# Kernel optimization log

Hardware: AMD Instinct MI355X
Metric: run time of the kernel (lower is better)

## Reference

```python
import jax, jax.numpy as jnp
import numpy as np

K = 8        # num capsules
DD = 64      # per-capsule dim (delta_d)
D = K * DD   # 512
T = 16384    # num target nodes (segments)
NB = 100000  # num neighbor nodes
E = 131072   # num edges
ROUIT = 3
BETA = 0.5


def seg_softmax(p, seg, num):
    # softmax over entries sharing the same segment id (axis 0)
    m = jax.lax.stop_gradient(jax.ops.segment_max(p, seg, num_segments=num))
    e = jnp.exp(p - m[seg])
    s = jax.ops.segment_sum(e, seg, num_segments=num)
    return e / s[seg]


def l2norm(x):
    # F.normalize along last axis with eps=1e-12
    n = jnp.sqrt(jnp.sum(x * x, axis=-1, keepdims=True))
    return x / jnp.maximum(n, 1e-12)


def setup_inputs() -> dict:
    key = jax.random.key(0)
    ks = jax.random.split(key, 9)
    return {
        "x_nb": jax.random.normal(ks[0], (NB, 512), dtype=jnp.float32),
        "ppr": jax.random.uniform(ks[1], (E,), dtype=jnp.float32),
        "pca_w": jax.random.normal(ks[2], (512, D), dtype=jnp.float32) * 0.02,
        "pca_b": jnp.zeros((D,), dtype=jnp.float32),
        "mlp_w": jax.random.normal(ks[3], (D, 40), dtype=jnp.float32) * 0.02,
        "mlp_b": jnp.zeros((40,), dtype=jnp.float32),
        "row_idx": jnp.sort(jax.random.randint(ks[4], (E,), 0, T, dtype=jnp.int32)),
        "col_idx": jax.random.randint(ks[5], (E,), 0, NB, dtype=jnp.int32),
        "x_idx": jax.random.randint(ks[6], (T,), 0, NB, dtype=jnp.int32),
    }


def reference(x_nb, ppr, pca_w, pca_b, mlp_w, mlp_b, row_idx, col_idx, x_idx):
    # pca projection + relu
    x = jax.nn.relu(x_nb @ pca_w + pca_b)            # (NB, D)
    # segment softmax of ppr over targets
    ppr = seg_softmax(ppr, row_idx, T)               # (E,)
    # is_xNorm: per-capsule l2 normalization
    x = l2norm(x.reshape(-1, K, DD)).reshape(-1, D)
    z = x[col_idx]                                   # (E, D) gathered neighbors
    zk = z.reshape(-1, K, DD)                        # (E, K, DD)
    # init_mtd == 2: ppr-weighted scatter-sum init
    u = jax.ops.segment_sum(z * ppr[:, None], row_idx, num_segments=T)  # (T, D)
    for it in range(ROUIT):
        uk = u[row_idx].reshape(-1, K, DD)           # (E, K, DD)
        p = jnp.einsum('ekd,ekd->ek', uk, zk)        # (E, K) capsule logits
        # attention == 1: segment softmax then blend with ppr
        p = seg_softmax(p, row_idx, T)
        p = BETA * p + (1.0 - BETA) * ppr[:, None]
        # final segment softmax
        p = seg_softmax(p, row_idx, T)
        u = jax.ops.segment_sum(zk * p[:, :, None], row_idx, num_segments=T)  # (T, K, DD)
        if it < ROUIT - 1:
            u = l2norm(u)
        u = u.reshape(T, D)
    out = jax.nn.relu(u)                             # dropout is identity at eval
    logits = out @ mlp_w + mlp_b                     # (T, nclass)
    return jax.nn.log_softmax(logits, axis=1)
```

## Files before the change

kernel.cpp:

```cpp
#include <hip/hip_runtime.h>
#include <cstdint>
#include <cstddef>

#define NB_N 100000
#define E_N  131072
#define T_N  16384
#define D_N  512
#define NCLS 40
#define NTILES 782
#define CAPR 12

typedef unsigned short u16;
typedef unsigned int   u32;
typedef __attribute__((ext_vector_type(8))) short  short8;
typedef __attribute__((ext_vector_type(4))) float  floatx4;

__device__ __forceinline__ u16 f2bf(float f) {
  u32 u = __float_as_uint(f);
  return (u16)((u + 0x7fffu + ((u >> 16) & 1u)) >> 16);
}
__device__ __forceinline__ void unpack8(uint4 z, float* f) {
  f[0] = __uint_as_float(z.x << 16);
  f[1] = __uint_as_float(z.x & 0xffff0000u);
  f[2] = __uint_as_float(z.y << 16);
  f[3] = __uint_as_float(z.y & 0xffff0000u);
  f[4] = __uint_as_float(z.z << 16);
  f[5] = __uint_as_float(z.z & 0xffff0000u);
  f[6] = __uint_as_float(z.w << 16);
  f[7] = __uint_as_float(z.w & 0xffff0000u);
}
__device__ __forceinline__ void gload_lds16(const void* g, void* s) {
  __builtin_amdgcn_global_load_lds(
      (const __attribute__((address_space(1))) unsigned int*)g,
      (__attribute__((address_space(3))) unsigned int*)s, 16, 0, 0);
}

__global__ void conv_bt(const float* __restrict__ w, u16* __restrict__ Bt) {
  int i = blockIdx.x * 256 + threadIdx.x;
  int n = i >> 9, k = i & 511;
  Bt[i] = f2bf(w[k * 512 + n]);
}

__global__ void conv_bt2(const float* __restrict__ w, u16* __restrict__ Bt2) {
  int i = blockIdx.x * 256 + threadIdx.x;
  int n = i >> 9, k = i & 511;
  Bt2[i] = (n < NCLS) ? f2bf(w[k * NCLS + n]) : (u16)0;
}

__global__ void conv_a(const float* __restrict__ A, u16* __restrict__ Ab) {
  int i = blockIdx.x * 256 + threadIdx.x;
  if (i >= NTILES * 128 * 128) return;
  int row = i >> 7;
  float4 v;
  if (row < NB_N) v = ((const float4*)(A + (size_t)row * 512))[i & 127];
  else            v = make_float4(0.f, 0.f, 0.f, 0.f);
  uint2 pk;
  pk.x = (u32)f2bf(v.x) | ((u32)f2bf(v.y) << 16);
  pk.y = (u32)f2bf(v.z) | ((u32)f2bf(v.w) << 16);
  *(uint2*)(Ab + (size_t)i * 4) = pk;
}

__global__ void build_offs(const int* __restrict__ rowi, int* __restrict__ offs) {
  int e = blockIdx.x * 256 + threadIdx.x;
  if (e >= E_N) return;
  int r  = rowi[e];
  int rp = (e == 0) ? -1 : rowi[e - 1];
  for (int t = rp + 1; t <= r; ++t) offs[t] = e;
  if (e == E_N - 1)
    for (int t = r + 1; t <= T_N; ++t) offs[t] = E_N;
}

__global__ void ppr_sm(const float* __restrict__ ppr, const int* __restrict__ offs,
                       float* __restrict__ pprn) {
  int t = blockIdx.x * 256 + threadIdx.x;
  int s = offs[t], en = offs[t + 1];
  if (s >= en) return;
  float m = -INFINITY;
  for (int e = s; e < en; ++e) m = fmaxf(m, ppr[e]);
  float sum = 0.f;
  for (int e = s; e < en; ++e) sum += expf(ppr[e] - m);
  float inv = 1.f / sum;
  for (int e = s; e < en; ++e) pprn[e] = expf(ppr[e] - m) * inv;
}

__global__ __launch_bounds__(256) void gemm_pca(
    const u16*   __restrict__ Ab,
    const u16*   __restrict__ Bt,
    const float* __restrict__ bias,
    u16*         __restrict__ xn) {
  __shared__ u16 SMEM[2 * 128 * 64];
  u16* As = SMEM;
  u16* Bs = SMEM + 128 * 64;
  const int tid  = threadIdx.x;
  const int wid  = tid >> 6, lane = tid & 63;
  const int quad = lane >> 4, l16 = lane & 15;
  const int b  = blockIdx.x;
  const int mt = (b & 7) | ((b >> 5) << 3);
  if (mt >= NTILES) return;
  const int m0 = mt * 128;
  const int n0 = ((b >> 3) & 3) * 128;
  const int wm = (wid >> 1) * 64;
  const int wn = (wid & 1) * 64;
  const int sw = l16 & 7;
  const u16* Arow = Ab + (size_t)m0 * 512;

  floatx4 acc[4][4];
#pragma unroll
  for (int i = 0; i < 4; ++i)
#pragma unroll
    for (int j = 0; j < 4; ++j) acc[i][j] = (floatx4){0.f, 0.f, 0.f, 0.f};

  for (int k0 = 0; k0 < 512; k0 += 64) {
#pragma unroll
    for (int j = 0; j < 4; ++j) {
      int ci  = j * 256 + wid * 64 + lane;
      int row = ci >> 3;
      int kcs = (lane & 7) ^ ((lane >> 3) & 7);
      gload_lds16(Arow + (size_t)row * 512 + k0 + kcs * 8,
                  &As[(size_t)(j * 256 + wid * 64) * 8]);
      gload_lds16(Bt + (size_t)(n0 + row) * 512 + k0 + kcs * 8,
                  &Bs[(size_t)(j * 256 + wid * 64) * 8]);
    }
    __syncthreads();
#pragma unroll
    for (int kk = 0; kk < 64; kk += 32) {
      short8 af[4], bf[4];
#pragma unroll
      for (int mi = 0; mi < 4; ++mi) {
        int c = (kk >> 3) + quad;
        af[mi] = *(const short8*)(&As[(wm + mi * 16 + l16) * 64 + ((c ^ sw) << 3)]);
      }
#pragma unroll
      for (int ni = 0; ni < 4; ++ni) {
        int c = (kk >> 3) + quad;
        bf[ni] = *(const short8*)(&Bs[(wn + ni * 16 + l16) * 64 + ((c ^ sw) << 3)]);
      }
#pragma unroll
      for (int mi = 0; mi < 4; ++mi)
#pragma unroll
        for (int ni = 0; ni < 4; ++ni)
          acc[mi][ni] = __builtin_amdgcn_mfma_f32_16x16x32_bf16(af[mi], bf[ni],
                                                                acc[mi][ni], 0, 0, 0);
    }
    __syncthreads();
  }

  u16* Os = SMEM;
#pragma unroll
  for (int mi = 0; mi < 4; ++mi) {
#pragma unroll
    for (int r = 0; r < 4; ++r) {
      int lrow = wm + mi * 16 + quad * 4 + r;
      float v[4];
      float ss = 0.f;
#pragma unroll
      for (int ni = 0; ni < 4; ++ni) {
        int n  = n0 + wn + ni * 16 + l16;
        float x = acc[mi][ni][r] + bias[n];
        x = fmaxf(x, 0.f);
        v[ni] = x;
        ss += x * x;
      }
      ss += __shfl_xor(ss, 1);
      ss += __shfl_xor(ss, 2);
      ss += __shfl_xor(ss, 4);
      ss += __shfl_xor(ss, 8);
      float sc = 1.f / fmaxf(sqrtf(ss), 1e-12f);
#pragma unroll
      for (int ni = 0; ni < 4; ++ni)
        Os[lrow * 128 + wn + ni * 16 + l16] = f2bf(v[ni] * sc);
    }
  }
  __syncthreads();
#pragma unroll
  for (int c8 = 0; c8 < 8; ++c8) {
    int idx = c8 * 256 + tid;
    int row = idx >> 4, chk = idx & 15;
    int gm = m0 + row;
    if (gm < NB_N) {
      uint4 val = *(const uint4*)(&Os[row * 128 + chk * 8]);
      *(uint4*)(xn + (size_t)gm * 512 + n0 + chk * 8) = val;
    }
  }
}

__global__ __launch_bounds__(256, 3) void fused_all(
    const u16* __restrict__ xn, const int* __restrict__ coli,
    const int* __restrict__ offs, const float* __restrict__ pprn,
    u16* __restrict__ ub) {
  const int lane = threadIdx.x & 63;
  const int t = blockIdx.x * 4 + (threadIdx.x >> 6);
  const int s = offs[t], en = offs[t + 1];
  int deg = en - s;
  if (deg > 64) deg = 64;
  const int cap = lane >> 3;
  const int slot = lane >> 3;

  int   mycol = (lane < deg) ? coli[s + lane] : 0;
  float myppr = (lane < deg) ? pprn[s + lane] : 0.f;

  uint4 zreg[CAPR];
#pragma unroll
  for (int j = 0; j < CAPR; ++j) {
    if (j < deg) {
      int c = __shfl(mycol, j);
      zreg[j] = *(const uint4*)(xn + (size_t)c * 512 + lane * 8);
    }
  }

  float uf[8] = {0.f, 0.f, 0.f, 0.f, 0.f, 0.f, 0.f, 0.f};
#pragma unroll
  for (int j = 0; j < CAPR; ++j) {
    if (j < deg) {
      float w = __shfl(myppr, j);
      float zf[8];
      unpack8(zreg[j], zf);
#pragma unroll
      for (int q = 0; q < 8; ++q) uf[q] += w * zf[q];
    }
  }
  for (int j = CAPR; j < deg; ++j) {
    float w = __shfl(myppr, j);
    int c = __shfl(mycol, j);
    uint4 zz = *(const uint4*)(xn + (size_t)c * 512 + lane * 8);
    float zf[8];
    unpack8(zz, zf);
#pragma unroll
    for (int q = 0; q < 8; ++q) uf[q] += w * zf[q];
  }

  float Preg[8];

  for (int it = 0; it < 3; ++it) {
#pragma unroll
    for (int j = 0; j < CAPR; ++j) {
      if (j < deg) {
        float zf[8];
        unpack8(zreg[j], zf);
        float d = uf[0]*zf[0] + uf[1]*zf[1] + uf[2]*zf[2] + uf[3]*zf[3] +
                  uf[4]*zf[4] + uf[5]*zf[5] + uf[6]*zf[6] + uf[7]*zf[7];
        d += __shfl_xor(d, 1);
        d += __shfl_xor(d, 2);
        d += __shfl_xor(d, 4);
        float dc = __shfl(d, (lane & 7) << 3);
        if (slot == (j & 7)) Preg[j >> 3] = dc;
      }
    }
    for (int j = CAPR; j < deg; ++j) {
      int c = __shfl(mycol, j);
      uint4 zz = *(const uint4*)(xn + (size_t)c * 512 + lane * 8);
      float zf[8];
      unpack8(zz, zf);
      float d = uf[0]*zf[0] + uf[1]*zf[1] + uf[2]*zf[2] + uf[3]*zf[3] +
                uf[4]*zf[4] + uf[5]*zf[5] + uf[6]*zf[6] + uf[7]*zf[7];
      d += __shfl_xor(d, 1);
      d += __shfl_xor(d, 2);
      d += __shfl_xor(d, 4);
      float dc = __shfl(d, (lane & 7) << 3);
      if (slot == (j & 7)) {
        int hi = j >> 3;
        if      (hi == 1) Preg[1] = dc;
        else if (hi == 2) Preg[2] = dc;
        else if (hi == 3) Preg[3] = dc;
        else if (hi == 4) Preg[4] = dc;
        else if (hi == 5) Preg[5] = dc;
        else if (hi == 6) Preg[6] = dc;
        else if (hi == 7) Preg[7] = dc;
      }
    }

    {
      float m1 = -INFINITY;
#pragma unroll
      for (int i = 0; i < 8; ++i)
        m1 = (slot + 8*i < deg) ? fmaxf(m1, Preg[i]) : m1;
      m1 = fmaxf(m1, __shfl_xor(m1, 8));
      m1 = fmaxf(m1, __shfl_xor(m1, 16));
      m1 = fmaxf(m1, __shfl_xor(m1, 32));
      float s1 = 0.f;
#pragma unroll
      for (int i = 0; i < 8; ++i)
        s1 += (slot + 8*i < deg) ? expf(Preg[i] - m1) : 0.f;
      s1 += __shfl_xor(s1, 8);
      s1 += __shfl_xor(s1, 16);
      s1 += __shfl_xor(s1, 32);
      float inv1 = 1.f / s1;
      float m2 = -INFINITY;
#pragma unroll
      for (int i = 0; i < 8; ++i) {
        int j = slot + 8*i;
        if (j < deg) {
          float pj = __shfl(myppr, j);
          float v = 0.5f * expf(Preg[i] - m1) * inv1 + 0.5f * pj;
          Preg[i] = v;
          m2 = fmaxf(m2, v);
        }
      }
      m2 = fmaxf(m2, __shfl_xor(m2, 8));
      m2 = fmaxf(m2, __shfl_xor(m2, 16));
      m2 = fmaxf(m2, __shfl_xor(m2, 32));
      float s2 = 0.f;
#pragma unroll
      for (int i = 0; i < 8; ++i)
        s2 += (slot + 8*i < deg) ? expf(Preg[i] - m2) : 0.f;
      s2 += __shfl_xor(s2, 8);
      s2 += __shfl_xor(s2, 16);
      s2 += __shfl_xor(s2, 32);
      float inv2 = 1.f / s2;
#pragma unroll
      for (int i = 0; i < 8; ++i)
        if (slot + 8*i < deg) Preg[i] = expf(Preg[i] - m2) * inv2;
    }

    float acc[8] = {0.f, 0.f, 0.f, 0.f, 0.f, 0.f, 0.f, 0.f};
#pragma unroll
    for (int j = 0; j < CAPR; ++j) {
      if (j < deg) {
        float w = __shfl(Preg[j >> 3], ((j & 7) << 3) | cap);
        float zf[8];
        unpack8(zreg[j], zf);
#pragma unroll
        for (int q = 0; q < 8; ++q) acc[q] += w * zf[q];
      }
    }
    for (int j = CAPR; j < deg; ++j) {
      int hi = j >> 3;
      float pr = Preg[1];
      if      (hi == 2) pr = Preg[2];
      else if (hi == 3) pr = Preg[3];
      else if (hi == 4) pr = Preg[4];
      else if (hi == 5) pr = Preg[5];
      else if (hi == 6) pr = Preg[6];
      else if (hi == 7) pr = Preg[7];
      float w = __shfl(pr, ((j & 7) << 3) | cap);
      int c = __shfl(mycol, j);
      uint4 zz = *(const uint4*)(xn + (size_t)c * 512 + lane * 8);
      float zf[8];
      unpack8(zz, zf);
#pragma unroll
      for (int q = 0; q < 8; ++q) acc[q] += w * zf[q];
    }
    if (it < 2) {
      float ss = 0.f;
#pragma unroll
      for (int q = 0; q < 8; ++q) ss += acc[q] * acc[q];
      ss += __shfl_xor(ss, 1);
      ss += __shfl_xor(ss, 2);
      ss += __shfl_xor(ss, 4);
      float sc = 1.f / fmaxf(sqrtf(ss), 1e-12f);
#pragma unroll
      for (int q = 0; q < 8; ++q) acc[q] *= sc;
    }
#pragma unroll
    for (int q = 0; q < 8; ++q) uf[q] = acc[q];
  }

  uint4 pk;
  pk.x = (u32)f2bf(fmaxf(uf[0], 0.f)) | ((u32)f2bf(fmaxf(uf[1], 0.f)) << 16);
  pk.y = (u32)f2bf(fmaxf(uf[2], 0.f)) | ((u32)f2bf(fmaxf(uf[3], 0.f)) << 16);
  pk.z = (u32)f2bf(fmaxf(uf[4], 0.f)) | ((u32)f2bf(fmaxf(uf[5], 0.f)) << 16);
  pk.w = (u32)f2bf(fmaxf(uf[6], 0.f)) | ((u32)f2bf(fmaxf(uf[7], 0.f)) << 16);
  *(uint4*)(ub + (size_t)t * 512 + lane * 8) = pk;
}

__global__ __launch_bounds__(256) void mlp_gemm(
    const u16* __restrict__ ub, const u16* __restrict__ Bt2,
    const float* __restrict__ mb, float* __restrict__ out) {
  const int wid = threadIdx.x >> 6, lane = threadIdx.x & 63;
  const int quad = lane >> 4, l16 = lane & 15;
  const int m0 = blockIdx.x * 64 + wid * 16;

  floatx4 acc[4];
#pragma unroll
  for (int ni = 0; ni < 4; ++ni) acc[ni] = (floatx4){0.f, 0.f, 0.f, 0.f};

#pragma unroll 4
  for (int kk = 0; kk < 512; kk += 32) {
    short8 af = *(const short8*)(ub + (size_t)(m0 + l16) * 512 + kk + quad * 8);
#pragma unroll
    for (int ni = 0; ni < 4; ++ni) {
      short8 bf = *(const short8*)(Bt2 + (size_t)(ni * 16 + l16) * 512 + kk + quad * 8);
      acc[ni] = __builtin_amdgcn_mfma_f32_16x16x32_bf16(af, bf, acc[ni], 0, 0, 0);
    }
  }

#pragma unroll
  for (int r = 0; r < 4; ++r) {
    int t = m0 + quad * 4 + r;
    float v[4];
    float mx = -INFINITY;
#pragma unroll
    for (int ni = 0; ni < 4; ++ni) {
      int c = ni * 16 + l16;
      float lg = (c < NCLS) ? (acc[ni][r] + mb[c]) : -INFINITY;
      v[ni] = lg;
      mx = fmaxf(mx, lg);
    }
    mx = fmaxf(mx, __shfl_xor(mx, 1));
    mx = fmaxf(mx, __shfl_xor(mx, 2));
    mx = fmaxf(mx, __shfl_xor(mx, 4));
    mx = fmaxf(mx, __shfl_xor(mx, 8));
    float se = 0.f;
#pragma unroll
    for (int ni = 0; ni < 4; ++ni) {
      int c = ni * 16 + l16;
      if (c < NCLS) se += expf(v[ni] - mx);
    }
    se += __shfl_xor(se, 1);
    se += __shfl_xor(se, 2);
    se += __shfl_xor(se, 4);
    se += __shfl_xor(se, 8);
    float lse = mx + logf(se);
#pragma unroll
    for (int ni = 0; ni < 4; ++ni) {
      int c = ni * 16 + l16;
      if (c < NCLS) out[(size_t)t * NCLS + c] = v[ni] - lse;
    }
  }
}

extern "C" void kernel_launch(void* const* d_in, const int* in_sizes, int n_in,
                              void* d_out, int out_size, void* d_ws, size_t ws_size,
                              hipStream_t stream) {
  const float* x_nb  = (const float*)d_in[0];
  const float* ppr   = (const float*)d_in[1];
  const float* pca_w = (const float*)d_in[2];
  const float* pca_b = (const float*)d_in[3];
  const float* mlp_w = (const float*)d_in[4];
  const float* mlp_b = (const float*)d_in[5];
  const int* row_idx = (const int*)d_in[6];
  const int* col_idx = (const int*)d_in[7];
  float* out = (float*)d_out;

  char* ws = (char*)d_ws;
  const size_t OFF_BT   = 0;
  const size_t OFF_PPRN = 512 * 1024;
  const size_t OFF_OFFS = 1024 * 1024;
  const size_t OFF_XN   = 1024 * 1024 + 128 * 1024;
  const size_t OFF_AB   = OFF_XN + (size_t)NB_N * 512 * 2;
  const size_t OFF_UB   = OFF_AB + (size_t)NTILES * 128 * 512 * 2;
  u16*   Bt   = (u16*)(ws + OFF_BT);
  u16*   Bt2  = (u16*)(ws + OFF_BT);
  float* pprn = (float*)(ws + OFF_PPRN);
  int*   offs = (int*)(ws + OFF_OFFS);
  u16*   xn   = (u16*)(ws + OFF_XN);
  u16*   Ab   = (u16*)(ws + OFF_AB);
  u16*   ub   = (u16*)(ws + OFF_UB);

  conv_bt<<<1024, 256, 0, stream>>>(pca_w, Bt);
  build_offs<<<512, 256, 0, stream>>>(row_idx, offs);
  ppr_sm<<<64, 256, 0, stream>>>(ppr, offs, pprn);

  conv_a<<<(NTILES * 128 * 128 + 255) / 256, 256, 0, stream>>>(x_nb, Ab);
  gemm_pca<<<98 * 32, 256, 0, stream>>>(Ab, Bt, pca_b, xn);
  conv_bt2<<<128, 256, 0, stream>>>(mlp_w, Bt2);

  fused_all<<<T_N / 4, 256, 0, stream>>>(xn, col_idx, offs, pprn, ub);

  mlp_gemm<<<256, 256, 0, stream>>>(ub, Bt2, mlp_b, out);
}
```

Before: 540.8 us.

## Run routing on per-capsule Gram matrices via MFMA for low-degree targets

For targets with at most 16 neighbors, the kernel now builds a per-capsule 16x16 Gram matrix of neighbor features with bf16 MFMA, stages it in LDS, and runs all three routing iterations as small matrix-vector products on coefficients. The norm of u is computed from the Gram matrix, so the final u is formed once from gathered z. This replaces repeated 64-dim dot products and weighted sums per iteration. High-degree targets keep the old path, and blocks shrink to two waves with LDS scratch. The Gram entries come from bf16 products, so rounding differs slightly, and the extra LDS use may limit occupancy.

```diff
diff --git a/kernel.cpp b/kernel.cpp
--- a/kernel.cpp
+++ b/kernel.cpp
@@ -184,175 +184,289 @@
   }
 }
 
-__global__ __launch_bounds__(256, 3) void fused_all(
+__device__ __forceinline__ void matvec16(const float (&g0)[16], const float (&g1)[16],
+                                         float w0, float w1, int base,
+                                         float& e0, float& e1) {
+  e0 = 0.f; e1 = 0.f;
+#pragma unroll
+  for (int j = 0; j < 8; ++j) {
+    float wj = __shfl(w0, base | j);
+    e0 += g0[j] * wj;
+    e1 += g1[j] * wj;
+  }
+#pragma unroll
+  for (int j = 0; j < 8; ++j) {
+    float wj = __shfl(w1, base | j);
+    e0 += g0[8 + j] * wj;
+    e1 += g1[8 + j] * wj;
+  }
+}
+
+__device__ __forceinline__ void segsm2(float& d0, float& d1, bool v0, bool v1) {
+  float m = fmaxf(v0 ? d0 : -INFINITY, v1 ? d1 : -INFINITY);
+  m = fmaxf(m, __shfl_xor(m, 1));
+  m = fmaxf(m, __shfl_xor(m, 2));
+  m = fmaxf(m, __shfl_xor(m, 4));
+  float e0 = v0 ? expf(d0 - m) : 0.f;
+  float e1 = v1 ? expf(d1 - m) : 0.f;
+  float s = e0 + e1;
+  s += __shfl_xor(s, 1);
+  s += __shfl_xor(s, 2);
+  s += __shfl_xor(s, 4);
+  float inv = 1.f / s;
+  d0 = e0 * inv;
+  d1 = e1 * inv;
+}
+
+__global__ __launch_bounds__(128, 4) void fused_all(
     const u16* __restrict__ xn, const int* __restrict__ coli,
     const int* __restrict__ offs, const float* __restrict__ pprn,
     u16* __restrict__ ub) {
+  __shared__ __align__(16) float Glds[2][8 * 260];
   const int lane = threadIdx.x & 63;
-  const int t = blockIdx.x * 4 + (threadIdx.x >> 6);
+  const int wv = threadIdx.x >> 6;
+  const int t = blockIdx.x * 2 + wv;
   const int s = offs[t], en = offs[t + 1];
   int deg = en - s;
   if (deg > 64) deg = 64;
-  const int cap = lane >> 3;
-  const int slot = lane >> 3;
 
   int   mycol = (lane < deg) ? coli[s + lane] : 0;
   float myppr = (lane < deg) ? pprn[s + lane] : 0.f;
 
-  uint4 zreg[CAPR];
-#pragma unroll
-  for (int j = 0; j < CAPR; ++j) {
-    if (j < deg) {
-      int c = __shfl(mycol, j);
-      zreg[j] = *(const uint4*)(xn + (size_t)c * 512 + lane * 8);
-    }
-  }
-
   float uf[8] = {0.f, 0.f, 0.f, 0.f, 0.f, 0.f, 0.f, 0.f};
-#pragma unroll
-  for (int j = 0; j < CAPR; ++j) {
-    if (j < deg) {
-      float w = __shfl(myppr, j);
-      float zf[8];
-      unpack8(zreg[j], zf);
-#pragma unroll
-      for (int q = 0; q < 8; ++q) uf[q] += w * zf[q];
-    }
-  }
-  for (int j = CAPR; j < deg; ++j) {
-    float w = __shfl(myppr, j);
-    int c = __shfl(mycol, j);
-    uint4 zz = *(const uint4*)(xn + (size_t)c * 512 + lane * 8);
-    float zf[8];
-    unpack8(zz, zf);
-#pragma unroll
-    for (int q = 0; q < 8; ++q) uf[q] += w * zf[q];
-  }
-
-  float Preg[8];
-
-  for (int it = 0; it < 3; ++it) {
+
+  if (deg <= 16) {
+    float* G = Glds[wv];
+    const int esrc = lane & 15, kq = lane >> 4;
+    int ce = __shfl(mycol, esrc);
+    const u16* zb = xn + (size_t)ce * 512 + kq * 8;
+    floatx4 gram[8];
+#pragma unroll
+    for (int c = 0; c < 8; ++c) {
+      short8 f0 = *(const short8*)(zb + c * 64);
+      short8 f1 = *(const short8*)(zb + c * 64 + 32);
+      floatx4 gg = (floatx4){0.f, 0.f, 0.f, 0.f};
+      gg = __builtin_amdgcn_mfma_f32_16x16x32_bf16(f0, f0, gg, 0, 0, 0);
+      gg = __builtin_amdgcn_mfma_f32_16x16x32_bf16(f1, f1, gg, 0, 0, 0);
+      gram[c] = gg;
+    }
+#pragma unroll
+    for (int c = 0; c < 8; ++c)
+      *(float4*)&G[c * 260 + esrc * 16 + kq * 4] = *(float4*)&gram[c];
+    const int cc = lane >> 3, i0 = lane & 7;
+    const int base = lane & 56;
+    float g0[16], g1[16];
+    {
+      const float* r0 = &G[cc * 260 + i0 * 16];
+      const float* r1 = &G[cc * 260 + (i0 + 8) * 16];
+#pragma unroll
+      for (int ch = 0; ch < 4; ++ch) {
+        float4 a = *(const float4*)(r0 + ch * 4);
+        float4 b = *(const float4*)(r1 + ch * 4);
+        g0[ch * 4 + 0] = a.x; g0[ch * 4 + 1] = a.y;
+        g0[ch * 4 + 2] = a.z; g0[ch * 4 + 3] = a.w;
+        g1[ch * 4 + 0] = b.x; g1[ch * 4 + 1] = b.y;
+        g1[ch * 4 + 2] = b.z; g1[ch * 4 + 3] = b.w;
+      }
+    }
+    const bool v0 = i0 < deg, v1 = (i0 + 8) < deg;
+    float pr0 = __shfl(myppr, i0);
+    float pr1 = __shfl(myppr, i0 + 8);
+
+    float d0, d1;
+    matvec16(g0, g1, pr0, pr1, base, d0, d1);
+
+    float w0 = 0.f, w1 = 0.f;
+#pragma unroll
+    for (int it = 0; it < 3; ++it) {
+      segsm2(d0, d1, v0, v1);
+      d0 = 0.5f * d0 + 0.5f * pr0;
+      d1 = 0.5f * d1 + 0.5f * pr1;
+      segsm2(d0, d1, v0, v1);
+      w0 = d0; w1 = d1;
+      if (it < 2) {
+        float e0, e1;
+        matvec16(g0, g1, w0, w1, base, e0, e1);
+        float nv = w0 * e0 + w1 * e1;
+        nv += __shfl_xor(nv, 1);
+        nv += __shfl_xor(nv, 2);
+        nv += __shfl_xor(nv, 4);
+        float invn = 1.f / fmaxf(sqrtf(nv), 1e-12f);
+        d0 = e0 * invn;
+        d1 = e1 * invn;
+      }
+    }
+
+#pragma unroll
+    for (int j = 0; j < 16; ++j) {
+      if (j < deg) {
+        float wj = __shfl((j < 8) ? w0 : w1, base | (j & 7));
+        int cj = __shfl(mycol, j);
+        uint4 zz = *(const uint4*)(xn + (size_t)cj * 512 + lane * 8);
+        float zf[8];
+        unpack8(zz, zf);
+#pragma unroll
+        for (int q = 0; q < 8; ++q) uf[q] += wj * zf[q];
+      }
+    }
+  } else {
+    const int cap = lane >> 3;
+    const int slot = lane >> 3;
+
+    uint4 zreg[CAPR];
 #pragma unroll
     for (int j = 0; j < CAPR; ++j) {
       if (j < deg) {
+        int c = __shfl(mycol, j);
+        zreg[j] = *(const uint4*)(xn + (size_t)c * 512 + lane * 8);
+      }
+    }
+
+#pragma unroll
+    for (int j = 0; j < CAPR; ++j) {
+      if (j < deg) {
+        float w = __shfl(myppr, j);
         float zf[8];
         unpack8(zreg[j], zf);
+#pragma unroll
+        for (int q = 0; q < 8; ++q) uf[q] += w * zf[q];
+      }
+    }
+    for (int j = CAPR; j < deg; ++j) {
+      float w = __shfl(myppr, j);
+      int c = __shfl(mycol, j);
+      uint4 zz = *(const uint4*)(xn + (size_t)c * 512 + lane * 8);
+      float zf[8];
+      unpack8(zz, zf);
+#pragma unroll
+      for (int q = 0; q < 8; ++q) uf[q] += w * zf[q];
+    }
+
+    float Preg[8];
+
+    for (int it = 0; it < 3; ++it) {
+#pragma unroll
+      for (int j = 0; j < CAPR; ++j) {
+        if (j < deg) {
+          float zf[8];
+          unpack8(zreg[j], zf);
+          float d = uf[0]*zf[0] + uf[1]*zf[1] + uf[2]*zf[2] + uf[3]*zf[3] +
+                    uf[4]*zf[4] + uf[5]*zf[5] + uf[6]*zf[6] + uf[7]*zf[7];
+          d += __shfl_xor(d, 1);
+          d += __shfl_xor(d, 2);
+          d += __shfl_xor(d, 4);
+          float dc = __shfl(d, (lane & 7) << 3);
+          if (slot == (j & 7)) Preg[j >> 3] = dc;
+        }
+      }
+      for (int j = CAPR; j < deg; ++j) {
+        int c = __shfl(mycol, j);
+        uint4 zz = *(const uint4*)(xn + (size_t)c * 512 + lane * 8);
+        float zf[8];
+        unpack8(zz, zf);
         float d = uf[0]*zf[0] + uf[1]*zf[1] + uf[2]*zf[2] + uf[3]*zf[3] +
                   uf[4]*zf[4] + uf[5]*zf[5] + uf[6]*zf[6] + uf[7]*zf[7];
         d += __shfl_xor(d, 1);
         d += __shfl_xor(d, 2);
         d += __shfl_xor(d, 4);
         float dc = __shfl(d, (lane & 7) << 3);
-        if (slot == (j & 7)) Preg[j >> 3] = dc;
-      }
-    }
-    for (int j = CAPR; j < deg; ++j) {
-      int c = __shfl(mycol, j);
-      uint4 zz = *(const uint4*)(xn + (size_t)c * 512 + lane * 8);
-      float zf[8];
-      unpack8(zz, zf);
-      float d = uf[0]*zf[0] + uf[1]*zf[1] + uf[2]*zf[2] + uf[3]*zf[3] +
-                uf[4]*zf[4] + uf[5]*zf[5] + uf[6]*zf[6] + uf[7]*zf[7];
-      d += __shfl_xor(d, 1);
-      d += __shfl_xor(d, 2);
-      d += __shfl_xor(d, 4);
-      float dc = __shfl(d, (lane & 7) << 3);
-      if (slot == (j & 7)) {
+        if (slot == (j & 7)) {
+          int hi = j >> 3;
+          if      (hi == 1) Preg[1] = dc;
+          else if (hi == 2) Preg[2] = dc;
+          else if (hi == 3) Preg[3] = dc;
+          else if (hi == 4) Preg[4] = dc;
+          else if (hi == 5) Preg[5] = dc;
+          else if (hi == 6) Preg[6] = dc;
+          else if (hi == 7) Preg[7] = dc;
+        }
+      }
+
+      {
+        float m1 = -INFINITY;
+#pragma unroll
+        for (int i = 0; i < 8; ++i)
+          m1 = (slot + 8*i < deg) ? fmaxf(m1, Preg[i]) : m1;
+        m1 = fmaxf(m1, __shfl_xor(m1, 8));
+        m1 = fmaxf(m1, __shfl_xor(m1, 16));
+        m1 = fmaxf(m1, __shfl_xor(m1, 32));
+        float s1 = 0.f;
+#pragma unroll
+        for (int i = 0; i < 8; ++i)
+          s1 += (slot + 8*i < deg) ? expf(Preg[i] - m1) : 0.f;
+        s1 += __shfl_xor(s1, 8);
+        s1 += __shfl_xor(s1, 16);
+        s1 += __shfl_xor(s1, 32);
+        float inv1 = 1.f / s1;
+        float m2 = -INFINITY;
+#pragma unroll
+        for (int i = 0; i < 8; ++i) {
+          int j = slot + 8*i;
+          if (j < deg) {
+            float pj = __shfl(myppr, j);
+            float v = 0.5f * expf(Preg[i] - m1) * inv1 + 0.5f * pj;
+            Preg[i] = v;
+            m2 = fmaxf(m2, v);
+          }
+        }
+        m2 = fmaxf(m2, __shfl_xor(m2, 8));
+        m2 = fmaxf(m2, __shfl_xor(m2, 16));
+        m2 = fmaxf(m2, __shfl_xor(m2, 32));
+        float s2 = 0.f;
+#pragma unroll
+        for (int i = 0; i < 8; ++i)
+          s2 += (slot + 8*i < deg) ? expf(Preg[i] - m2) : 0.f;
+        s2 += __shfl_xor(s2, 8);
+        s2 += __shfl_xor(s2, 16);
+        s2 += __shfl_xor(s2, 32);
+        float inv2 = 1.f / s2;
+#pragma unroll
+        for (int i = 0; i < 8; ++i)
+          if (slot + 8*i < deg) Preg[i] = expf(Preg[i] - m2) * inv2;
+      }
+
+      float acc[8] = {0.f, 0.f, 0.f, 0.f, 0.f, 0.f, 0.f, 0.f};
+#pragma unroll
+      for (int j = 0; j < CAPR; ++j) {
+        if (j < deg) {
+          float w = __shfl(Preg[j >> 3], ((j & 7) << 3) | cap);
+          float zf[8];
+          unpack8(zreg[j], zf);
+#pragma unroll
+          for (int q = 0; q < 8; ++q) acc[q] += w * zf[q];
+        }
+      }
+      for (int j = CAPR; j < deg; ++j) {
         int hi = j >> 3;
-        if      (hi == 1) Preg[1] = dc;
-        else if (hi == 2) Preg[2] = dc;
-        else if (hi == 3) Preg[3] = dc;
-        else if (hi == 4) Preg[4] = dc;
-        else if (hi == 5) Preg[5] = dc;
-        else if (hi == 6) Preg[6] = dc;
-        else if (hi == 7) Preg[7] = dc;
-      }
-    }
-
-    {
-      float m1 = -INFINITY;
-#pragma unroll
-      for (int i = 0; i < 8; ++i)
-        m1 = (slot + 8*i < deg) ? fmaxf(m1, Preg[i]) : m1;
-      m1 = fmaxf(m1, __shfl_xor(m1, 8));
-      m1 = fmaxf(m1, __shfl_xor(m1, 16));
-      m1 = fmaxf(m1, __shfl_xor(m1, 32));
-      float s1 = 0.f;
-#pragma unroll
-      for (int i = 0; i < 8; ++i)
-        s1 += (slot + 8*i < deg) ? expf(Preg[i] - m1) : 0.f;
-      s1 += __shfl_xor(s1, 8);
-      s1 += __shfl_xor(s1, 16);
-      s1 += __shfl_xor(s1, 32);
-      float inv1 = 1.f / s1;
-      float m2 = -INFINITY;
-#pragma unroll
-      for (int i = 0; i < 8; ++i) {
-        int j = slot + 8*i;
-        if (j < deg) {
-          float pj = __shfl(myppr, j);
-          float v = 0.5f * expf(Preg[i] - m1) * inv1 + 0.5f * pj;
-          Preg[i] = v;
-          m2 = fmaxf(m2, v);
-        }
-      }
-      m2 = fmaxf(m2, __shfl_xor(m2, 8));
-      m2 = fmaxf(m2, __shfl_xor(m2, 16));
-      m2 = fmaxf(m2, __shfl_xor(m2, 32));
-      float s2 = 0.f;
-#pragma unroll
-      for (int i = 0; i < 8; ++i)
-        s2 += (slot + 8*i < deg) ? expf(Preg[i] - m2) : 0.f;
-      s2 += __shfl_xor(s2, 8);
-      s2 += __shfl_xor(s2, 16);
-      s2 += __shfl_xor(s2, 32);
-      float inv2 = 1.f / s2;
-#pragma unroll
-      for (int i = 0; i < 8; ++i)
-        if (slot + 8*i < deg) Preg[i] = expf(Preg[i] - m2) * inv2;
-    }
-
-    float acc[8] = {0.f, 0.f, 0.f, 0.f, 0.f, 0.f, 0.f, 0.f};
-#pragma unroll
-    for (int j = 0; j < CAPR; ++j) {
-      if (j < deg) {
-        float w = __shfl(Preg[j >> 3], ((j & 7) << 3) | cap);
+        float pr = Preg[1];
+        if      (hi == 2) pr = Preg[2];
+        else if (hi == 3) pr = Preg[3];
+        else if (hi == 4) pr = Preg[4];
+        else if (hi == 5) pr = Preg[5];
+        else if (hi == 6) pr = Preg[6];
+        else if (hi == 7) pr = Preg[7];
+        float w = __shfl(pr, ((j & 7) << 3) | cap);
+        int c = __shfl(mycol, j);
+        uint4 zz = *(const uint4*)(xn + (size_t)c * 512 + lane * 8);
         float zf[8];
-        unpack8(zreg[j], zf);
+        unpack8(zz, zf);
 #pragma unroll
         for (int q = 0; q < 8; ++q) acc[q] += w * zf[q];
       }
-    }
-    for (int j = CAPR; j < deg; ++j) {
-      int hi = j >> 3;
-      float pr = Preg[1];
-      if      (hi == 2) pr = Preg[2];
-      else if (hi == 3) pr = Preg[3];
-      else if (hi == 4) pr = Preg[4];
-      else if (hi == 5) pr = Preg[5];
-      else if (hi == 6) pr = Preg[6];
-      else if (hi == 7) pr = Preg[7];
-      float w = __shfl(pr, ((j & 7) << 3) | cap);
-      int c = __shfl(mycol, j);
-      uint4 zz = *(const uint4*)(xn + (size_t)c * 512 + lane * 8);
-      float zf[8];
-      unpack8(zz, zf);
-#pragma unroll
-      for (int q = 0; q < 8; ++q) acc[q] += w * zf[q];
-    }
-    if (it < 2) {
-      float ss = 0.f;
-#pragma unroll
-      for (int q = 0; q < 8; ++q) ss += acc[q] * acc[q];
-      ss += __shfl_xor(ss, 1);
-      ss += __shfl_xor(ss, 2);
-      ss += __shfl_xor(ss, 4);
-      float sc = 1.f / fmaxf(sqrtf(ss), 1e-12f);
-#pragma unroll
-      for (int q = 0; q < 8; ++q) acc[q] *= sc;
-    }
-#pragma unroll
-    for (int q = 0; q < 8; ++q) uf[q] = acc[q];
+      if (it < 2) {
+        float ss = 0.f;
+#pragma unroll
+        for (int q = 0; q < 8; ++q) ss += acc[q] * acc[q];
+        ss += __shfl_xor(ss, 1);
+        ss += __shfl_xor(ss, 2);
+        ss += __shfl_xor(ss, 4);
+        float sc = 1.f / fmaxf(sqrtf(ss), 1e-12f);
+#pragma unroll
+        for (int q = 0; q < 8; ++q) acc[q] *= sc;
+      }
+#pragma unroll
+      for (int q = 0; q < 8; ++q) uf[q] = acc[q];
+    }
   }
 
   uint4 pk;
@@ -455,7 +569,7 @@
   gemm_pca<<<98 * 32, 256, 0, stream>>>(Ab, Bt, pca_b, xn);
   conv_bt2<<<128, 256, 0, stream>>>(mlp_w, Bt2);
 
-  fused_all<<<T_N / 4, 256, 0, stream>>>(xn, col_idx, offs, pprn, ub);
+  fused_all<<<T_N / 2, 128, 0, stream>>>(xn, col_idx, offs, pprn, ub);
 
   mlp_gemm<<<256, 256, 0, stream>>>(ub, Bt2, mlp_b, out);
 }
```

After: 507.1 us. 1.07x faster.
